# Performance work log

Hardware: AMD Instinct MI355X
Metric: run time of the kernel (lower is better)

## Reference

```python
import jax, jax.numpy as jnp
import numpy as np

B, NH, S, H = 4, 8, 1024, 128
I = 512
E = 8
K = 2
EPS = 1e-5


def setup_inputs() -> dict:
    key = jax.random.key(0)
    ks = jax.random.split(key, 11)
    sH = 1.0 / np.sqrt(H)
    sI = 1.0 / np.sqrt(I)
    return {
        "x": jax.random.normal(ks[0], (B, NH, S, H), dtype=jnp.float32),
        "gate_w": jax.random.uniform(ks[1], (E, H), jnp.float32, -sH, sH),
        "gate_b": jax.random.uniform(ks[2], (E,), jnp.float32, -sH, sH),
        "ln1_g": jnp.ones((E, H), jnp.float32),
        "ln1_b": jnp.zeros((E, H), jnp.float32),
        "w1": jax.random.uniform(ks[3], (E, I, H), jnp.float32, -sH, sH),
        "ln2_g": jnp.ones((E, I), jnp.float32),
        "ln2_b": jnp.zeros((E, I), jnp.float32),
        "w2": jax.random.uniform(ks[4], (E, H, I), jnp.float32, -sI, sI),
        "b2": jax.random.uniform(ks[5], (E, H), jnp.float32, -sI, sI),
    }


def _ln_normalize(x):
    mu = jnp.mean(x, axis=-1, keepdims=True)
    var = jnp.mean(jnp.square(x - mu), axis=-1, keepdims=True)
    return (x - mu) * jax.lax.rsqrt(var + EPS)


def reference(x, gate_w, gate_b, ln1_g, ln1_b, w1, ln2_g, ln2_b, w2, b2):
    orig_shape = x.shape
    x_flat = x.reshape(-1, H)  # [N, H]

    # gate: softmax over experts, then top-k
    logits = x_flat @ gate_w.T + gate_b  # [N, E]
    probs = jax.nn.softmax(logits, axis=-1)
    topk_scores, topk_idx = jax.lax.top_k(probs, K)  # [N, K]

    # per-expert MLP (dropout is identity in eval). Normalization of x is
    # expert-independent; affine params differ per expert.
    xn = _ln_normalize(x_flat)  # [N, H]
    h1 = xn[None, :, :] * ln1_g[:, None, :] + ln1_b[:, None, :]  # [E, N, H]
    a1 = jax.nn.gelu(h1, approximate=False)
    t = jnp.einsum("enh,eih->eni", a1, w1)  # [E, N, I]
    h2 = _ln_normalize(t) * ln2_g[:, None, :] + ln2_b[:, None, :]
    a2 = jax.nn.gelu(h2, approximate=False)
    expert_out = jnp.einsum("eni,ehi->enh", a2, w2) + b2[:, None, :]  # [E, N, H]

    # combine weights: sum top-k scores into dense [N, E]
    combine = jnp.sum(jax.nn.one_hot(topk_idx, E, dtype=x.dtype) * topk_scores[..., None], axis=1)
    out = jnp.einsum("ne,enh->nh", combine, expert_out)
    return out.reshape(orig_shape)
```

## Files before the change

kernel.cpp:

```cpp
#include <hip/hip_runtime.h>
#include <hip/hip_bf16.h>

#define N_TOK 32768
#define H 128
#define I_DIM 512
#define E 8
#define EPS 1e-5f
#define GATE_TPB 128
#define NSLOT_MAX (N_TOK * 2 + E * 32)

typedef __attribute__((ext_vector_type(8))) short short8;
typedef __attribute__((ext_vector_type(4))) float f32x4;
typedef __attribute__((ext_vector_type(2))) unsigned int u32x2;
typedef __attribute__((ext_vector_type(4))) unsigned int u32x4;
typedef __attribute__((ext_vector_type(8))) __bf16 bf16x8;

__device__ inline unsigned short f2bf(float f){
  unsigned int u = __builtin_bit_cast(unsigned int, f);
  u += 0x7fffu + ((u >> 16) & 1u);
  return (unsigned short)(u >> 16);
}
__device__ inline float bf2f(unsigned short s){
  unsigned int u = ((unsigned int)s) << 16;
  return __builtin_bit_cast(float, u);
}
__device__ inline unsigned int cvtpk(float lo, float hi){
  __hip_bfloat162 h = __float22bfloat162_rn(make_float2(lo, hi));
  unsigned int r;
  __builtin_memcpy(&r, &h, 4);
  return r;
}
__device__ inline float gelu_fast(float x){
  const float A = 0.10294517f;
  const float B = 2.30214175f;
  float x2 = x * x;
  float v  = __builtin_fmaf(x2, A, B);
  float z  = __builtin_amdgcn_exp2f(v * x);
  float r  = __builtin_amdgcn_rcpf(z + 1.f);
  return __builtin_fmaf(-x, r, x);
}
__device__ inline f32x4 mfma16(short8 a, short8 b, f32x4 c){
  return __builtin_amdgcn_mfma_f32_16x16x32_bf16(
      __builtin_bit_cast(bf16x8, a), __builtin_bit_cast(bf16x8, b), c, 0, 0, 0);
}

__device__ inline int slot_to_expert(const int* __restrict__ cnt, int slot0,
                                     int& base, int& ne){
  int e = -1, p = 0;
  #pragma unroll
  for (int q = 0; q < E; ++q){
    int c = cnt[q];
    int pc = (c + 31) & ~31;
    if (slot0 >= p && slot0 < p + pc){ e = q; base = slot0 - p; ne = c; }
    p += pc;
  }
  return e;
}

__global__ __launch_bounds__(256) void k_front(
    const float* __restrict__ w1, const float* __restrict__ w2,
    unsigned short* __restrict__ w1p, unsigned short* __restrict__ w2p,
    const float* __restrict__ x, const float* __restrict__ gw,
    const float* __restrict__ gb, unsigned short* __restrict__ xn,
    int* __restrict__ cnt, int* __restrict__ list, float* __restrict__ score,
    float* __restrict__ out){
  __shared__ __align__(16) float gws[E * H];
  __shared__ float gbs[E];
  __shared__ int   lcnt[E];
  __shared__ int   gbase[E];
  __shared__ int   te[2][GATE_TPB];
  __shared__ float tsc[2][GATE_TPB];
  __shared__ int   tlp[2][GATE_TPB];

  int tid = threadIdx.x;
  int blk = blockIdx.x;

  if (blk >= 512){
    float4 z = {0.f, 0.f, 0.f, 0.f};
    float4* o4 = (float4*)out;
    int base4 = (blk - 512) * 2048 + tid;
    #pragma unroll
    for (int q = 0; q < 8; ++q) o4[base4 + q * 256] = z;
    return;
  }

  if (blk < 256){
    int q = blk * 256 + tid;
    int e = q >> 13, rem = q & 8191;
    {
      int it = rem >> 8, kt = (rem >> 6) & 3, l = rem & 63;
      int row = it * 16 + (l & 15), h0 = kt * 32 + (l >> 4) * 8;
      const float* src = w1 + ((size_t)(e * 512 + row) * 128 + h0);
      float4 v0 = *(const float4*)src, v1 = *(const float4*)(src + 4);
      short8 o;
      #pragma unroll
      for (int j = 0; j < 4; ++j){ o[j] = (short)f2bf(v0[j]); o[j+4] = (short)f2bf(v1[j]); }
      *(short8*)(w1p + (size_t)q * 8) = o;
    }
    {
      int ht = rem >> 10, kt = (rem >> 6) & 15, l = rem & 63;
      int row = ht * 16 + (l & 15), i0 = kt * 32 + (l >> 4) * 8;
      const float* src = w2 + ((size_t)(e * 128 + row) * 512 + i0);
      float4 v0 = *(const float4*)src, v1 = *(const float4*)(src + 4);
      short8 o;
      #pragma unroll
      for (int j = 0; j < 4; ++j){ o[j] = (short)f2bf(v0[j]); o[j+4] = (short)f2bf(v1[j]); }
      *(short8*)(w2p + (size_t)q * 8) = o;
    }
    return;
  }

  for (int i = tid; i < E * H; i += 256) gws[i] = gw[i];
  if (tid < E){ gbs[tid] = gb[tid]; lcnt[tid] = 0; }
  __syncthreads();

  int wave = tid >> 6, lane = tid & 63;
  int g = lane >> 3, c8 = lane & 7;
  int tok0 = (blk - 256) * GATE_TPB;
  const float4* gws4 = (const float4*)gws;

  for (int t = 0; t < 4; ++t){
    int lt = t * 32 + wave * 8 + g;
    int tok = tok0 + lt;
    const float4* xr = (const float4*)(x + (size_t)tok * H) + c8 * 4;
    float4 v[4];
    #pragma unroll
    for (int q = 0; q < 4; ++q) v[q] = xr[q];

    float S = 0.f, Q = 0.f;
    float lg[E];
    #pragma unroll
    for (int e = 0; e < E; e++) lg[e] = 0.f;
    #pragma unroll
    for (int q = 0; q < 4; ++q){
      #pragma unroll
      for (int r = 0; r < 4; ++r){
        float f = v[q][r];
        S += f; Q = __builtin_fmaf(f, f, Q);
      }
      #pragma unroll
      for (int e = 0; e < E; e++){
        float4 wv = gws4[e * 32 + c8 * 4 + q];
        #pragma unroll
        for (int r = 0; r < 4; ++r) lg[e] = __builtin_fmaf(v[q][r], wv[r], lg[e]);
      }
    }
    #pragma unroll
    for (int m = 1; m < 8; m <<= 1){
      S += __shfl_xor(S, m);
      Q += __shfl_xor(Q, m);
      #pragma unroll
      for (int e = 0; e < E; e++) lg[e] += __shfl_xor(lg[e], m);
    }

    float mu = S * (1.f / H);
    float var = Q * (1.f / H) - mu * mu;
    float rsig = rsqrtf(fmaxf(var, 0.f) + EPS);

    short8 s0, s1;
    #pragma unroll
    for (int r = 0; r < 4; ++r){
      s0[r]     = (short)f2bf((v[0][r] - mu) * rsig);
      s0[r + 4] = (short)f2bf((v[1][r] - mu) * rsig);
      s1[r]     = (short)f2bf((v[2][r] - mu) * rsig);
      s1[r + 4] = (short)f2bf((v[3][r] - mu) * rsig);
    }
    unsigned short* xo = xn + (size_t)tok * H + c8 * 16;
    *(short8*)xo = s0;
    *(short8*)(xo + 8) = s1;

    if (c8 == 0){
      float mx = -1e30f;
      #pragma unroll
      for (int e = 0; e < E; e++){ lg[e] += gbs[e]; mx = fmaxf(mx, lg[e]); }
      float p[E], sum = 0.f;
      #pragma unroll
      for (int e = 0; e < E; e++){ p[e] = __expf(lg[e] - mx); sum += p[e]; }
      float inv = 1.f / sum;
      int e0 = 0; float p0 = p[0];
      #pragma unroll
      for (int e = 1; e < E; e++) if (p[e] > p0){ e0 = e; p0 = p[e]; }
      int e1 = -1; float p1 = -1.f;
      #pragma unroll
      for (int e = 0; e < E; e++) if (e != e0 && p[e] > p1){ e1 = e; p1 = p[e]; }
      te[0][lt] = e0; tsc[0][lt] = p0 * inv; tlp[0][lt] = atomicAdd(&lcnt[e0], 1);
      te[1][lt] = e1; tsc[1][lt] = p1 * inv; tlp[1][lt] = atomicAdd(&lcnt[e1], 1);
    }
  }
  __syncthreads();
  if (tid < E) gbase[tid] = atomicAdd(&cnt[tid], lcnt[tid]);
  __syncthreads();
  if (tid < GATE_TPB){
    int tok = tok0 + tid;
    #pragma unroll
    for (int k2 = 0; k2 < 2; k2++){
      int ee = te[k2][tid];
      int pos = gbase[ee] + tlp[k2][tid];
      list[ee * N_TOK + pos] = tok;
      score[ee * N_TOK + pos] = tsc[k2][tid];
    }
  }
}

__global__ __launch_bounds__(256, 2) void k_mlp(
    const unsigned short* __restrict__ xn,
    const float* __restrict__ ln1g, const float* __restrict__ ln1b,
    const unsigned short* __restrict__ w1p,
    const float* __restrict__ ln2g, const float* __restrict__ ln2b,
    const unsigned short* __restrict__ w2p, const float* __restrict__ b2,
    const int* __restrict__ cnt, const int* __restrict__ list,
    const float* __restrict__ score, float* __restrict__ out){
  __shared__ __align__(16) unsigned short tls[2][16 * I_DIM];
  __shared__ float2 psum[4][2][16];
  __shared__ __align__(16) float pg2[I_DIM], pb2[I_DIM];
  __shared__ float pbb[H];

  int tid = threadIdx.x, wv = tid >> 6, lane = tid & 63;
  int slot0 = blockIdx.x * 32;
  int base, ne;
  int e = slot_to_expert(cnt, slot0, base, ne);
  if (e < 0 || base >= ne) return;
  const int l15 = lane & 15, l4 = lane >> 4;

  pg2[tid]       = ln2g[e * I_DIM + tid];
  pg2[tid + 256] = ln2g[e * I_DIM + tid + 256];
  pb2[tid]       = ln2b[e * I_DIM + tid];
  pb2[tid + 256] = ln2b[e * I_DIM + tid + 256];
  if (tid < H) pbb[tid] = b2[e * H + tid];

  {
    const float* g1e = ln1g + e * H;
    const float* b1e = ln1b + e * H;
    #pragma unroll
    for (int c2 = 0; c2 < 2; ++c2){
      int combo = wv * 2 + c2;
      int kt = combo >> 1, tl = combo & 1;
      int h0 = kt * 32 + l4 * 8;
      int s = base + tl * 16 + l15;
      int tok = s < ne ? list[e * N_TOK + s] : 0;
      short8 xv = *(const short8*)(xn + (size_t)tok * H + h0);
      float4 ga = *(const float4*)(g1e + h0), gbv = *(const float4*)(g1e + h0 + 4);
      float4 ba = *(const float4*)(b1e + h0), bbv = *(const float4*)(b1e + h0 + 4);
      float q[8];
      #pragma unroll
      for (int j = 0; j < 8; ++j){
        float f = bf2f((unsigned short)xv[j]);
        float gg = j < 4 ? ga[j] : gbv[j - 4];
        float bb_ = j < 4 ? ba[j] : bbv[j - 4];
        q[j] = gelu_fast(__builtin_fmaf(f, gg, bb_));
      }
      u32x4 vw;
      vw[0] = cvtpk(q[0], q[1]); vw[1] = cvtpk(q[2], q[3]);
      vw[2] = cvtpk(q[4], q[5]); vw[3] = cvtpk(q[6], q[7]);
      *(u32x4*)((char*)&tls[0][0] + (size_t)((combo * 64 + lane) << 4)) = vw;
    }
  }
  __syncthreads();
  short8 b1f[4][2];
  #pragma unroll
  for (int kt = 0; kt < 4; ++kt)
    #pragma unroll
    for (int tl = 0; tl < 2; ++tl)
      b1f[kt][tl] = *(const short8*)((const char*)&tls[0][0] +
                                     (size_t)(((kt * 2 + tl) * 64 + lane) << 4));
  __syncthreads();

  const unsigned short* w1e = w1p + ((size_t)e << 16);
  float Sx[2] = {0.f, 0.f}, Qx[2] = {0.f, 0.f};

  short8 afA[4], afB[4];
  {
    int it = wv * 8;
    #pragma unroll
    for (int kt = 0; kt < 4; ++kt)
      afA[kt] = *(const short8*)(w1e + (size_t)(((it << 2) | kt) << 9) + lane * 8);
  }
  #pragma unroll
  for (int ii = 0; ii < 8; ++ii){
    int it = wv * 8 + ii;
    if (ii < 7){
      int itn = it + 1;
      #pragma unroll
      for (int kt = 0; kt < 4; ++kt)
        afB[kt] = *(const short8*)(w1e + (size_t)(((itn << 2) | kt) << 9) + lane * 8);
    }
    __builtin_amdgcn_sched_barrier(0);
    f32x4 acc[2];
    #pragma unroll
    for (int tl = 0; tl < 2; ++tl){ f32x4 z = {0.f,0.f,0.f,0.f}; acc[tl] = z; }
    __builtin_amdgcn_s_setprio(1);
    #pragma unroll
    for (int kt = 0; kt < 4; ++kt)
      #pragma unroll
      for (int tl = 0; tl < 2; ++tl)
        acc[tl] = mfma16(afA[kt], b1f[kt][tl], acc[tl]);
    __builtin_amdgcn_s_setprio(0);

    int kt2 = it >> 1;
    int lh = (it * 2 + (l4 >> 1)) & 3;
    int off = ((kt2 * 4 + lh) * 16 + l15) * 8 + (l4 & 1) * 4;
    #pragma unroll
    for (int tl = 0; tl < 2; ++tl){
      #pragma unroll
      for (int r = 0; r < 4; ++r){
        float v = acc[tl][r];
        Sx[tl] += v; Qx[tl] = __builtin_fmaf(v, v, Qx[tl]);
      }
      u32x2 w0;
      w0[0] = cvtpk(acc[tl][0], acc[tl][1]);
      w0[1] = cvtpk(acc[tl][2], acc[tl][3]);
      *(u32x2*)((char*)&tls[tl][0] + (size_t)off * 2) = w0;
    }
    #pragma unroll
    for (int kt = 0; kt < 4; ++kt) afA[kt] = afB[kt];
  }

  #pragma unroll
  for (int tl = 0; tl < 2; ++tl){
    Sx[tl] += __shfl_xor(Sx[tl], 16);  Qx[tl] += __shfl_xor(Qx[tl], 16);
    Sx[tl] += __shfl_xor(Sx[tl], 32);  Qx[tl] += __shfl_xor(Qx[tl], 32);
  }
  if (l4 == 0){
    #pragma unroll
    for (int tl = 0; tl < 2; ++tl)
      psum[wv][tl][l15] = make_float2(Sx[tl], Qx[tl]);
  }
  __syncthreads();

  {
    int tl3 = wv & 1, ktb = (wv >> 1) * 8;
    float S = 0.f, Q = 0.f;
    #pragma unroll
    for (int w4 = 0; w4 < 4; ++w4){
      float2 p = psum[w4][tl3][l15];
      S += p.x; Q += p.y;
    }
    float mu = S * (1.f / I_DIM);
    float var = __builtin_fmaf(Q, 1.f / I_DIM, -mu * mu);
    float rsig = rsqrtf(fmaxf(var, 0.f) + EPS);
    float mrs = mu * rsig;

    unsigned short* ta = &tls[tl3][0];
    #pragma unroll
    for (int k2 = 0; k2 < 8; ++k2){
      int kt = ktb + k2;
      int i0 = kt * 32 + l4 * 8;
      float4 g2a = *(const float4*)(pg2 + i0), g2b = *(const float4*)(pg2 + i0 + 4);
      float4 b2a = *(const float4*)(pb2 + i0), b2b = *(const float4*)(pb2 + i0 + 4);
      short8 tv = *(const short8*)((const char*)ta + (size_t)(kt * 64 + lane) * 16);
      float q[8];
      #pragma unroll
      for (int j = 0; j < 8; ++j){
        float gg = j < 4 ? g2a[j] : g2b[j - 4];
        float bb_ = j < 4 ? b2a[j] : b2b[j - 4];
        float v0 = __builtin_fmaf(bf2f((unsigned short)tv[j]), rsig, -mrs);
        q[j] = gelu_fast(__builtin_fmaf(v0, gg, bb_));
      }
      u32x4 vw;
      vw[0] = cvtpk(q[0], q[1]); vw[1] = cvtpk(q[2], q[3]);
      vw[2] = cvtpk(q[4], q[5]); vw[3] = cvtpk(q[6], q[7]);
      *(u32x4*)((char*)ta + (size_t)(kt * 64 + lane) * 16) = vw;
    }
  }
  __syncthreads();

  const unsigned short* w2e = w2p + ((size_t)e << 16);
  f32x4 c[2][2];
  #pragma unroll
  for (int hh = 0; hh < 2; ++hh)
    #pragma unroll
    for (int tl = 0; tl < 2; ++tl){ f32x4 z = {0.f,0.f,0.f,0.f}; c[hh][tl] = z; }

  short8 awA[2], awB[2], fA[2], fB[2];
  {
    #pragma unroll
    for (int hh = 0; hh < 2; ++hh){
      int h = wv * 2 + hh;
      awA[hh] = *(const short8*)(w2e + (size_t)(((h << 4) | 0) << 9) + lane * 8);
    }
    #pragma unroll
    for (int tl = 0; tl < 2; ++tl)
      fA[tl] = *(const short8*)((const char*)&tls[tl][0] + (size_t)(0 * 64 + lane) * 16);
  }
  #pragma unroll
  for (int kt = 0; kt < 16; ++kt){
    if (kt < 15){
      int ktn = kt + 1;
      #pragma unroll
      for (int hh = 0; hh < 2; ++hh){
        int h = wv * 2 + hh;
        awB[hh] = *(const short8*)(w2e + (size_t)(((h << 4) | ktn) << 9) + lane * 8);
      }
      #pragma unroll
      for (int tl = 0; tl < 2; ++tl)
        fB[tl] = *(const short8*)((const char*)&tls[tl][0] + (size_t)(ktn * 64 + lane) * 16);
    }
    __builtin_amdgcn_sched_barrier(0);
    __builtin_amdgcn_s_setprio(1);
    #pragma unroll
    for (int tl = 0; tl < 2; ++tl){
      c[0][tl] = mfma16(fA[tl], awA[0], c[0][tl]);
      c[1][tl] = mfma16(fA[tl], awA[1], c[1][tl]);
    }
    __builtin_amdgcn_s_setprio(0);
    #pragma unroll
    for (int hh = 0; hh < 2; ++hh) awA[hh] = awB[hh];
    #pragma unroll
    for (int tl = 0; tl < 2; ++tl) fA[tl] = fB[tl];
  }

  float bb[2];
  #pragma unroll
  for (int hh = 0; hh < 2; ++hh) bb[hh] = pbb[(wv * 2 + hh) * 16 + l15];

  #pragma unroll
  for (int tl = 0; tl < 2; ++tl){
    #pragma unroll
    for (int r = 0; r < 4; ++r){
      int s = base + tl * 16 + l4 * 4 + r;
      if (s < ne){
        int tok = list[e * N_TOK + s];
        float sc = score[e * N_TOK + s];
        float* orow = out + (size_t)tok * H + l15;
        #pragma unroll
        for (int hh = 0; hh < 2; ++hh)
          atomicAdd(orow + (wv * 2 + hh) * 16, (c[hh][tl][r] + bb[hh]) * sc);
      }
    }
  }
}

extern "C" void kernel_launch(void* const* d_in, const int* in_sizes, int n_in,
                              void* d_out, int out_size, void* d_ws, size_t ws_size,
                              hipStream_t stream){
  const float* x     = (const float*)d_in[0];
  const float* gw    = (const float*)d_in[1];
  const float* gb    = (const float*)d_in[2];
  const float* ln1g  = (const float*)d_in[3];
  const float* ln1b  = (const float*)d_in[4];
  const float* w1    = (const float*)d_in[5];
  const float* ln2g  = (const float*)d_in[6];
  const float* ln2b  = (const float*)d_in[7];
  const float* w2    = (const float*)d_in[8];
  const float* b2    = (const float*)d_in[9];
  float* out = (float*)d_out;

  char* w = (char*)d_ws;
  unsigned short* xn  = (unsigned short*)w;  w += (size_t)N_TOK * H * 2;
  unsigned short* w1p = (unsigned short*)w;  w += (size_t)E * I_DIM * H * 2;
  unsigned short* w2p = (unsigned short*)w;  w += (size_t)E * H * I_DIM * 2;
  int*    list  = (int*)w;                   w += (size_t)E * N_TOK * 4;
  float*  score = (float*)w;                 w += (size_t)E * N_TOK * 4;
  int*    cnt   = (int*)w;                   w += 256;

  (void)hipMemsetAsync(cnt, 0, 256, stream);

  k_front<<<dim3(1024), dim3(256), 0, stream>>>(
      w1, w2, w1p, w2p, x, gw, gb, xn, cnt, list, score, out);
  k_mlp<<<dim3(NSLOT_MAX / 32), dim3(256), 0, stream>>>(
      xn, ln1g, ln1b, w1p, ln2g, ln2b, w2p, b2, cnt, list, score, out);
}
```

Measured before the change: 73.23 us.

## Precompute per-expert LN1+GELU activations in gate kernel, scatter into expert-sorted buffer

The gate kernel now keeps normalized tokens in swizzled shared memory. After slot assignment it applies each chosen expert's LN1 affine and GELU, then writes bf16 activations directly into an expert-sorted buffer at the token's slot position. The MLP kernel then loads its B fragments contiguously from this buffer instead of gathering by token index, transforming, and round-tripping through LDS with two barriers. The cost is twice the intermediate write traffic (two experts per token) and higher LDS use in the front kernel, which may lower its occupancy.

```diff
diff --git a/kernel.cpp b/kernel.cpp
--- a/kernel.cpp
+++ b/kernel.cpp
@@ -61,10 +61,15 @@
     const float* __restrict__ w1, const float* __restrict__ w2,
     unsigned short* __restrict__ w1p, unsigned short* __restrict__ w2p,
     const float* __restrict__ x, const float* __restrict__ gw,
-    const float* __restrict__ gb, unsigned short* __restrict__ xn,
+    const float* __restrict__ gb,
+    const float* __restrict__ ln1g, const float* __restrict__ ln1b,
+    unsigned short* __restrict__ a1buf,
     int* __restrict__ cnt, int* __restrict__ list, float* __restrict__ score,
     float* __restrict__ out){
   __shared__ __align__(16) float gws[E * H];
+  __shared__ __align__(16) float g1s[E * H];
+  __shared__ __align__(16) float b1s[E * H];
+  __shared__ __align__(16) unsigned short xnl[GATE_TPB * H];
   __shared__ float gbs[E];
   __shared__ int   lcnt[E];
   __shared__ int   gbase[E];
@@ -110,7 +115,9 @@
     return;
   }
 
-  for (int i = tid; i < E * H; i += 256) gws[i] = gw[i];
+  for (int i = tid; i < E * H; i += 256){
+    gws[i] = gw[i]; g1s[i] = ln1g[i]; b1s[i] = ln1b[i];
+  }
   if (tid < E){ gbs[tid] = gb[tid]; lcnt[tid] = 0; }
   __syncthreads();
 
@@ -165,9 +172,10 @@
       s1[r]     = (short)f2bf((v[2][r] - mu) * rsig);
       s1[r + 4] = (short)f2bf((v[3][r] - mu) * rsig);
     }
-    unsigned short* xo = xn + (size_t)tok * H + c8 * 16;
-    *(short8*)xo = s0;
-    *(short8*)(xo + 8) = s1;
+    int swz = (lt & 7) << 4;
+    char* xrow = (char*)xnl + lt * 256;
+    *(short8*)(xrow + ((c8 * 32) ^ swz))      = s0;
+    *(short8*)(xrow + ((c8 * 32 + 16) ^ swz)) = s1;
 
     if (c8 == 0){
       float mx = -1e30f;
@@ -190,21 +198,45 @@
   __syncthreads();
   if (tid < E) gbase[tid] = atomicAdd(&cnt[tid], lcnt[tid]);
   __syncthreads();
-  if (tid < GATE_TPB){
-    int tok = tok0 + tid;
-    #pragma unroll
-    for (int k2 = 0; k2 < 2; k2++){
-      int ee = te[k2][tid];
-      int pos = gbase[ee] + tlp[k2][tid];
-      list[ee * N_TOK + pos] = tok;
-      score[ee * N_TOK + pos] = tsc[k2][tid];
+
+  {
+    int lt = tid >> 1, half = tid & 1;
+    int swz = (lt & 7) << 4;
+    const char* xrow = (const char*)xnl + lt * 256;
+    #pragma unroll
+    for (int k2 = 0; k2 < 2; ++k2){
+      int ee = te[k2][lt];
+      int pos = gbase[ee] + tlp[k2][lt];
+      if (half == 0){
+        list[ee * N_TOK + pos] = tok0 + lt;
+        score[ee * N_TOK + pos] = tsc[k2][lt];
+      }
+      const float* g1r = g1s + ee * H + half * 64;
+      const float* b1r = b1s + ee * H + half * 64;
+      unsigned short* dst = a1buf + ((size_t)ee * N_TOK + pos) * H + half * 64;
+      #pragma unroll
+      for (int hc = 0; hc < 64; hc += 8){
+        short8 xv = *(const short8*)(xrow + (((half * 64 + hc) * 2) ^ swz));
+        float4 ga = *(const float4*)(g1r + hc), gb4 = *(const float4*)(g1r + hc + 4);
+        float4 ba = *(const float4*)(b1r + hc), bb4 = *(const float4*)(b1r + hc + 4);
+        float q[8];
+        #pragma unroll
+        for (int j = 0; j < 8; ++j){
+          float gg = j < 4 ? ga[j] : gb4[j - 4];
+          float bb_ = j < 4 ? ba[j] : bb4[j - 4];
+          q[j] = gelu_fast(__builtin_fmaf(bf2f((unsigned short)xv[j]), gg, bb_));
+        }
+        u32x4 vw;
+        vw[0] = cvtpk(q[0], q[1]); vw[1] = cvtpk(q[2], q[3]);
+        vw[2] = cvtpk(q[4], q[5]); vw[3] = cvtpk(q[6], q[7]);
+        *(u32x4*)(dst + hc) = vw;
+      }
     }
   }
 }
 
 __global__ __launch_bounds__(256, 2) void k_mlp(
-    const unsigned short* __restrict__ xn,
-    const float* __restrict__ ln1g, const float* __restrict__ ln1b,
+    const unsigned short* __restrict__ a1buf,
     const unsigned short* __restrict__ w1p,
     const float* __restrict__ ln2g, const float* __restrict__ ln2b,
     const unsigned short* __restrict__ w2p, const float* __restrict__ b2,
@@ -228,42 +260,14 @@
   pb2[tid + 256] = ln2b[e * I_DIM + tid + 256];
   if (tid < H) pbb[tid] = b2[e * H + tid];
 
-  {
-    const float* g1e = ln1g + e * H;
-    const float* b1e = ln1b + e * H;
-    #pragma unroll
-    for (int c2 = 0; c2 < 2; ++c2){
-      int combo = wv * 2 + c2;
-      int kt = combo >> 1, tl = combo & 1;
-      int h0 = kt * 32 + l4 * 8;
-      int s = base + tl * 16 + l15;
-      int tok = s < ne ? list[e * N_TOK + s] : 0;
-      short8 xv = *(const short8*)(xn + (size_t)tok * H + h0);
-      float4 ga = *(const float4*)(g1e + h0), gbv = *(const float4*)(g1e + h0 + 4);
-      float4 ba = *(const float4*)(b1e + h0), bbv = *(const float4*)(b1e + h0 + 4);
-      float q[8];
-      #pragma unroll
-      for (int j = 0; j < 8; ++j){
-        float f = bf2f((unsigned short)xv[j]);
-        float gg = j < 4 ? ga[j] : gbv[j - 4];
-        float bb_ = j < 4 ? ba[j] : bbv[j - 4];
-        q[j] = gelu_fast(__builtin_fmaf(f, gg, bb_));
-      }
-      u32x4 vw;
-      vw[0] = cvtpk(q[0], q[1]); vw[1] = cvtpk(q[2], q[3]);
-      vw[2] = cvtpk(q[4], q[5]); vw[3] = cvtpk(q[6], q[7]);
-      *(u32x4*)((char*)&tls[0][0] + (size_t)((combo * 64 + lane) << 4)) = vw;
-    }
-  }
-  __syncthreads();
   short8 b1f[4][2];
   #pragma unroll
-  for (int kt = 0; kt < 4; ++kt)
-    #pragma unroll
-    for (int tl = 0; tl < 2; ++tl)
-      b1f[kt][tl] = *(const short8*)((const char*)&tls[0][0] +
-                                     (size_t)(((kt * 2 + tl) * 64 + lane) << 4));
-  __syncthreads();
+  for (int tl = 0; tl < 2; ++tl){
+    const unsigned short* ar = a1buf + ((size_t)e * N_TOK + base + tl * 16 + l15) * H;
+    #pragma unroll
+    for (int kt = 0; kt < 4; ++kt)
+      b1f[kt][tl] = *(const short8*)(ar + kt * 32 + l4 * 8);
+  }
 
   const unsigned short* w1e = w1p + ((size_t)e << 16);
   float Sx[2] = {0.f, 0.f}, Qx[2] = {0.f, 0.f};
@@ -446,17 +450,17 @@
   float* out = (float*)d_out;
 
   char* w = (char*)d_ws;
-  unsigned short* xn  = (unsigned short*)w;  w += (size_t)N_TOK * H * 2;
-  unsigned short* w1p = (unsigned short*)w;  w += (size_t)E * I_DIM * H * 2;
-  unsigned short* w2p = (unsigned short*)w;  w += (size_t)E * H * I_DIM * 2;
-  int*    list  = (int*)w;                   w += (size_t)E * N_TOK * 4;
-  float*  score = (float*)w;                 w += (size_t)E * N_TOK * 4;
-  int*    cnt   = (int*)w;                   w += 256;
+  unsigned short* a1buf = (unsigned short*)w;  w += ((size_t)E * N_TOK + 64) * H * 2;
+  unsigned short* w1p = (unsigned short*)w;    w += (size_t)E * I_DIM * H * 2;
+  unsigned short* w2p = (unsigned short*)w;    w += (size_t)E * H * I_DIM * 2;
+  int*    list  = (int*)w;                     w += (size_t)E * N_TOK * 4;
+  float*  score = (float*)w;                   w += (size_t)E * N_TOK * 4;
+  int*    cnt   = (int*)w;                     w += 256;
 
   (void)hipMemsetAsync(cnt, 0, 256, stream);
 
   k_front<<<dim3(1024), dim3(256), 0, stream>>>(
-      w1, w2, w1p, w2p, x, gw, gb, xn, cnt, list, score, out);
+      w1, w2, w1p, w2p, x, gw, gb, ln1g, ln1b, a1buf, cnt, list, score, out);
   k_mlp<<<dim3(NSLOT_MAX / 32), dim3(256), 0, stream>>>(
-      xn, ln1g, ln1b, w1p, ln2g, ln2b, w2p, b2, cnt, list, score, out);
-}
+      a1buf, w1p, ln2g, ln2b, w2p, b2, cnt, list, score, out);
+}
```

New measurement: 77.78 us. 1.06x slower.
